# Performance work log

Measured on AMD Instinct MI355X. Metric: run time of the kernel, lower is better.

## Reference

```python
import jax, jax.numpy as jnp
import numpy as np

N, E, LE = 200000, 1000000, 1000000
ND, ED = 128, 128
EPS = 1e-5


def layer_norm(v, g, b):
    m = v.mean(-1, keepdims=True)
    var = ((v - m) ** 2).mean(-1, keepdims=True)
    return (v - m) * jax.lax.rsqrt(var + EPS) * g + b


def setup_inputs() -> dict:
    key = jax.random.key(0)
    ks = jax.random.split(key, 12)
    s = 0.02
    return {
        "x": jax.random.normal(ks[0], (N, ND), jnp.float32),
        "edge_attr": jax.random.normal(ks[1], (E, ED), jnp.float32),
        "lg_x": jax.random.normal(ks[2], (E, ED), jnp.float32),
        "lg_edge_attr": jax.random.normal(ks[3], (LE, 1), jnp.float32),
        "W_line": jax.random.normal(ks[4], (2 * ED + 1, ED), jnp.float32) * s,
        "b_line": jnp.zeros((ED,), jnp.float32),
        "W_gate": jax.random.normal(ks[5], (ED, ED), jnp.float32) * s,
        "b_gate": jnp.zeros((ED,), jnp.float32),
        "W_atom": jax.random.normal(ks[6], (ND + ED, ND), jnp.float32) * s,
        "b_atom": jnp.zeros((ND,), jnp.float32),
        "g_node": jnp.ones((ND,), jnp.float32),
        "beta_node": jnp.zeros((ND,), jnp.float32),
        "g_edge": jnp.ones((ED,), jnp.float32),
        "beta_edge": jnp.zeros((ED,), jnp.float32),
        "edge_index": jax.random.randint(ks[7], (2, E), 0, N, jnp.int64),
        "lg_edge_index": jax.random.randint(ks[8], (2, LE), 0, E, jnp.int64),
    }


def reference(x, edge_attr, lg_x, lg_edge_attr, W_line, b_line, W_gate, b_gate,
              W_atom, b_atom, g_node, beta_node, g_edge, beta_edge,
              edge_index, lg_edge_index):
    n_lg = lg_x.shape[0]  # == E (line-graph nodes are bonds)
    lg_src, lg_dst = lg_edge_index[0], lg_edge_index[1]
    # 1) LineGraphConv: gather-concat-MLP-scatter(mean)
    msg = jnp.concatenate([lg_x[lg_src], lg_x[lg_dst], lg_edge_attr], axis=-1)  # [LE, 2*ED+1]
    msg = jax.nn.silu(msg @ W_line + b_line)  # [LE, ED]
    agg_sum = jax.ops.segment_sum(msg, lg_dst, num_segments=n_lg)
    cnt = jax.ops.segment_sum(jnp.ones((lg_dst.shape[0], 1), msg.dtype), lg_dst, num_segments=n_lg)
    lg_x_new = lg_x + agg_sum / jnp.maximum(cnt, 1.0)  # scatter-mean, empty segs -> 0
    # 2) EdgeGateUpdate
    edge_attr_new = layer_norm(edge_attr + lg_x_new, g_edge, beta_edge)
    gate = jax.nn.sigmoid(edge_attr_new @ W_gate + b_gate)
    # 3) AtomGraphConv: gated scatter(sum) into atoms
    col = edge_index[1]
    agg = jax.ops.segment_sum(gate * edge_attr_new, col, num_segments=x.shape[0])  # [N, ED]
    h = jax.nn.silu(jnp.concatenate([x, agg], axis=-1) @ W_atom + b_atom)
    x_new = layer_norm(x + h, g_node, beta_node)
    return x_new, edge_attr_new, lg_x_new
```

## Files before the change

### kernel.cpp

```cpp
#include <hip/hip_runtime.h>


typedef __attribute__((ext_vector_type(8))) short s16x8;
typedef __attribute__((ext_vector_type(4))) float f32x4;

#define SCAN_CHUNK 2048

__device__ __forceinline__ short f2bf(float f) {
    unsigned u = __float_as_uint(f);
    u += 0x7FFF + ((u >> 16) & 1);
    return (short)(u >> 16);
}
__device__ __forceinline__ float bf2f(unsigned short h) {
    return __uint_as_float(((unsigned)h) << 16);
}
__device__ __forceinline__ s16x8 pack8(const float* v) {
    s16x8 r;
    #pragma unroll
    for (int j = 0; j < 8; ++j) r[j] = f2bf(v[j]);
    return r;
}

__global__ __launch_bounds__(256) void k_pack(const float* __restrict__ W,
                                              short* __restrict__ P, int nchunk) {
    int c = blockIdx.x * 256 + threadIdx.x;
    if (c >= nchunk) return;
    int g = c >> 7, col = c & 127, k0 = g * 8;
    s16x8 v;
    #pragma unroll
    for (int j = 0; j < 8; ++j) v[j] = f2bf(W[(size_t)(k0 + j) * 128 + col]);
    ((s16x8*)P)[c] = v;
}

__global__ __launch_bounds__(256) void k_cvt(const float* __restrict__ x,
                                             short* __restrict__ y, long n8) {
    long i = (long)blockIdx.x * 256 + threadIdx.x;
    const long stride = (long)gridDim.x * 256;
    for (; i < n8; i += stride) {
        float buf[8];
        *(float4*)&buf[0] = ((const float4*)x)[2 * i];
        *(float4*)&buf[4] = ((const float4*)x)[2 * i + 1];
        ((s16x8*)y)[i] = pack8(buf);
    }
}

__global__ __launch_bounds__(256) void k_hist(const int* __restrict__ idx,
                                              int* __restrict__ deg, int n) {
    int i = blockIdx.x * 256 + threadIdx.x;
    if (i < n) atomicAdd(&deg[idx[i]], 1);
}

__global__ __launch_bounds__(256) void k_scan_block(const int* __restrict__ in, int n,
                                                    int* __restrict__ out,
                                                    int* __restrict__ bsum) {
    __shared__ int ts[256];
    const int b = blockIdx.x, t = threadIdx.x;
    const int base = b * SCAN_CHUNK + t * 8;
    int v[8]; int s = 0;
    #pragma unroll
    for (int i = 0; i < 8; ++i) { v[i] = (base + i < n) ? in[base + i] : 0; s += v[i]; }
    ts[t] = s;
    __syncthreads();
    int x = s;
    for (int off = 1; off < 256; off <<= 1) {
        int y = (t >= off) ? ts[t - off] : 0;
        __syncthreads();
        x += y; ts[t] = x;
        __syncthreads();
    }
    if (t == 255) bsum[b] = x;
    int run = x - s;
    #pragma unroll
    for (int i = 0; i < 8; ++i) {
        if (base + i < n) out[base + i] = run;
        run += v[i];
    }
}

__global__ void k_scan_bsum(int* __restrict__ bsum, int nb) {
    const int lane = threadIdx.x;
    int carry = 0;
    for (int base = 0; base < nb; base += 64) {
        int i = base + lane;
        int v = (i < nb) ? bsum[i] : 0;
        int inc = v;
        #pragma unroll
        for (int off = 1; off < 64; off <<= 1) {
            int t = __shfl_up(inc, off);
            if (lane >= off) inc += t;
        }
        if (i < nb) bsum[i] = inc - v + carry;
        carry += __shfl(inc, 63);
    }
}

__global__ __launch_bounds__(256) void k_scan_add(int* __restrict__ off,
                                                  const int* __restrict__ bsum,
                                                  int n, int nedge) {
    int i = blockIdx.x * 256 + threadIdx.x;
    if (i < n) off[i] += bsum[i / SCAN_CHUNK];
    if (i == 0) off[n] = nedge;
}

__global__ __launch_bounds__(256) void k_fill_pos(const int* __restrict__ idx,
                                                  const int* __restrict__ off,
                                                  int* __restrict__ cur,
                                                  int* __restrict__ pos, int n) {
    int i = blockIdx.x * 256 + threadIdx.x;
    if (i < n) {
        int s = idx[i];
        int p = atomicAdd(&cur[s], 1);
        pos[i] = off[s] + p;
    }
}

__global__ __launch_bounds__(256) void k_line_csr(
    const short* __restrict__ lgx_bf, const float* __restrict__ lg_ea,
    const short* __restrict__ Wp, const float* __restrict__ W_line,
    const float* __restrict__ b_line,
    const int* __restrict__ lg_src, const int* __restrict__ lg_dst,
    const int* __restrict__ pos_lg,
    short* __restrict__ msg, int LEn)
{
    __shared__ __align__(16) short sh[128][136];
    const int tid = threadIdx.x;
    const int ln = tid & 63, wv = tid >> 6;
    const int l15 = ln & 15, lhi = ln >> 4;
    const int eb = blockIdx.x * 128 + wv * 32;
    const s16x8* Bv = (const s16x8*)Wp;

    const short *sp[2], *dp[2];
    #pragma unroll
    for (int mt = 0; mt < 2; ++mt) {
        int e = eb + mt * 16 + l15;
        int ec = e < LEn ? e : LEn - 1;
        sp[mt] = lgx_bf + (size_t)lg_src[ec] * 128;
        dp[mt] = lgx_bf + (size_t)lg_dst[ec] * 128;
    }

    f32x4 acc[2][8];
    #pragma unroll
    for (int m = 0; m < 2; ++m)
        #pragma unroll
        for (int n = 0; n < 8; ++n) acc[m][n] = (f32x4){0.f, 0.f, 0.f, 0.f};

    #pragma unroll 2
    for (int kt = 0; kt < 8; ++kt) {
        int ko = (kt & 3) * 32 + lhi * 8;
        s16x8 a[2];
        #pragma unroll
        for (int mt = 0; mt < 2; ++mt)
            a[mt] = *(const s16x8*)(((kt < 4) ? sp[mt] : dp[mt]) + ko);
        const s16x8* brow = Bv + (size_t)(kt * 4 + lhi) * 128 + l15;
        #pragma unroll
        for (int nt = 0; nt < 8; ++nt) {
            s16x8 b = brow[nt * 16];
            acc[0][nt] = __builtin_amdgcn_mfma_f32_16x16x32_bf16(a[0], b, acc[0][nt], 0, 0, 0);
            acc[1][nt] = __builtin_amdgcn_mfma_f32_16x16x32_bf16(a[1], b, acc[1][nt], 0, 0, 0);
        }
    }

    float eav[2][4];
    #pragma unroll
    for (int mt = 0; mt < 2; ++mt)
        #pragma unroll
        for (int r = 0; r < 4; ++r) {
            int e = eb + mt * 16 + lhi * 4 + r;
            eav[mt][r] = lg_ea[e < LEn ? e : 0];
        }

    #pragma unroll
    for (int nt = 0; nt < 8; ++nt) {
        int col = nt * 16 + l15;
        float wl = W_line[(size_t)256 * 128 + col];
        float bs = b_line[col];
        #pragma unroll
        for (int mt = 0; mt < 2; ++mt)
            #pragma unroll
            for (int r = 0; r < 4; ++r) {
                float v = acc[mt][nt][r] + bs + wl * eav[mt][r];
                float s = v / (1.f + __expf(-v));
                sh[wv * 32 + mt * 16 + lhi * 4 + r][col] = f2bf(s);
            }
    }
    __syncthreads();
    #pragma unroll
    for (int i = 0; i < 8; ++i) {
        int c = tid + i * 256;
        int row = c >> 4, q = c & 15;
        int e = blockIdx.x * 128 + row;
        if (e < LEn) {
            int p = pos_lg[e];
            *(s16x8*)&msg[(size_t)p * 128 + q * 8] = *(const s16x8*)&sh[row][q * 8];
        }
    }
}

__global__ __launch_bounds__(256) void k_lg_edge_fused(
    const short* __restrict__ msg, const float* __restrict__ lg_x,
    const float* __restrict__ edge_attr, const int* __restrict__ off,
    const float* __restrict__ g_edge, const float* __restrict__ beta_edge,
    float* __restrict__ out_lg, float* __restrict__ out_edge,
    short* __restrict__ enew_bf, int En)
{
    const int wave = threadIdx.x >> 6, lane = threadIdx.x & 63;
    const int e = blockIdx.x * 4 + wave;
    if (e >= En) return;
    const int o0 = off[e], o1 = off[e + 1];
    const int cnt = o1 - o0;
    const short* base = msg + (size_t)o0 * 128 + lane * 2;
    float s0 = 0.f, s1 = 0.f;
    int j = 0;
    for (; j + 1 < cnt; j += 2) {
        ushort2 u0 = *(const ushort2*)(base + (size_t)j * 128);
        ushort2 u1 = *(const ushort2*)(base + (size_t)(j + 1) * 128);
        s0 += bf2f(u0.x) + bf2f(u1.x);
        s1 += bf2f(u0.y) + bf2f(u1.y);
    }
    if (j < cnt) {
        ushort2 u = *(const ushort2*)(base + (size_t)j * 128);
        s0 += bf2f(u.x); s1 += bf2f(u.y);
    }
    const float inv = 1.f / fmaxf((float)cnt, 1.f);
    const size_t rb = (size_t)e * 128 + lane * 2;
    float2 lx = *(const float2*)&lg_x[rb];
    float l0 = fmaf(s0, inv, lx.x), l1 = fmaf(s1, inv, lx.y);
    *(float2*)&out_lg[rb] = make_float2(l0, l1);

    float2 ea = *(const float2*)&edge_attr[rb];
    float t0 = ea.x + l0, t1 = ea.y + l1;
    float s = t0 + t1, sq = t0 * t0 + t1 * t1;
    #pragma unroll
    for (int o = 32; o; o >>= 1) {
        s  += __shfl_xor(s, o);
        sq += __shfl_xor(sq, o);
    }
    float mean = s * (1.f / 128.f);
    float var  = sq * (1.f / 128.f) - mean * mean;
    float r = rsqrtf(var + 1e-5f);
    int j0 = lane * 2;
    float e0 = (t0 - mean) * r * g_edge[j0]     + beta_edge[j0];
    float e1 = (t1 - mean) * r * g_edge[j0 + 1] + beta_edge[j0 + 1];
    *(float2*)&out_edge[rb] = make_float2(e0, e1);
    if (enew_bf) {
        ushort2 ub = make_ushort2((unsigned short)f2bf(e0), (unsigned short)f2bf(e1));
        *(ushort2*)&enew_bf[rb] = ub;
    }
}

__global__ __launch_bounds__(256) void k_lg_gather(
    const short* __restrict__ msg, const float* __restrict__ lg_x,
    const int* __restrict__ off, float* __restrict__ out_lg, int En)
{
    const int wave = threadIdx.x >> 6, lane = threadIdx.x & 63;
    const int e = blockIdx.x * 4 + wave;
    if (e >= En) return;
    const int o0 = off[e], o1 = off[e + 1];
    const int cnt = o1 - o0;
    const short* base = msg + (size_t)o0 * 128 + lane * 2;
    float s0 = 0.f, s1 = 0.f;
    for (int j = 0; j < cnt; ++j) {
        ushort2 u = *(const ushort2*)(base + (size_t)j * 128);
        s0 += bf2f(u.x); s1 += bf2f(u.y);
    }
    const float inv = 1.f / fmaxf((float)cnt, 1.f);
    const size_t rb = (size_t)e * 128 + lane * 2;
    float2 lx = *(const float2*)&lg_x[rb];
    *(float2*)&out_lg[rb] = make_float2(fmaf(s0, inv, lx.x), fmaf(s1, inv, lx.y));
}

__global__ __launch_bounds__(256) void k_edge_ln(
    const float* __restrict__ lnew, const float* __restrict__ edge_attr,
    const float* __restrict__ g_edge, const float* __restrict__ beta_edge,
    float* __restrict__ out_edge, int En)
{
    const int wave = threadIdx.x >> 6, lane = threadIdx.x & 63;
    const int e = blockIdx.x * 4 + wave;
    if (e >= En) return;
    const size_t rb = (size_t)e * 128 + lane * 2;
    float2 lv = *(const float2*)&lnew[rb];
    float2 ea = *(const float2*)&edge_attr[rb];
    float t0 = ea.x + lv.x, t1 = ea.y + lv.y;
    float s = t0 + t1, sq = t0 * t0 + t1 * t1;
    #pragma unroll
    for (int o = 32; o; o >>= 1) { s += __shfl_xor(s, o); sq += __shfl_xor(sq, o); }
    float mean = s * (1.f / 128.f);
    float var  = sq * (1.f / 128.f) - mean * mean;
    float r = rsqrtf(var + 1e-5f);
    int j0 = lane * 2;
    float o0 = (t0 - mean) * r * g_edge[j0]     + beta_edge[j0];
    float o1 = (t1 - mean) * r * g_edge[j0 + 1] + beta_edge[j0 + 1];
    *(float2*)&out_edge[rb] = make_float2(o0, o1);
}

template <bool BF>
__global__ __launch_bounds__(256) void k_gate_csr(
    const short* __restrict__ EinB, const float* __restrict__ EinF,
    const short* __restrict__ Wp, const float* __restrict__ bg,
    const int* __restrict__ pos_at, short* __restrict__ gated, int En)
{
    __shared__ __align__(16) short sh[128][136];
    const int tid = threadIdx.x;
    const int ln = tid & 63, wv = tid >> 6;
    const int l15 = ln & 15, lhi = ln >> 4;
    const int eb = blockIdx.x * 128 + wv * 32;
    const s16x8* Bv = (const s16x8*)Wp;

    int rowi[2];
    #pragma unroll
    for (int mt = 0; mt < 2; ++mt) {
        int e = eb + mt * 16 + l15;
        rowi[mt] = e < En ? e : En - 1;
    }

    f32x4 acc[2][8];
    #pragma unroll
    for (int m = 0; m < 2; ++m)
        #pragma unroll
        for (int n = 0; n < 8; ++n) acc[m][n] = (f32x4){0.f, 0.f, 0.f, 0.f};

    #pragma unroll 2
    for (int kt = 0; kt < 4; ++kt) {
        int ko = kt * 32 + lhi * 8;
        s16x8 a[2];
        #pragma unroll
        for (int mt = 0; mt < 2; ++mt) {
            if (BF) {
                a[mt] = *(const s16x8*)(EinB + (size_t)rowi[mt] * 128 + ko);
            } else {
                const float* p = EinF + (size_t)rowi[mt] * 128 + ko;
                float buf[8];
                *(float4*)&buf[0] = *(const float4*)p;
                *(float4*)&buf[4] = *(const float4*)(p + 4);
                a[mt] = pack8(buf);
            }
        }
        const s16x8* brow = Bv + (size_t)(kt * 4 + lhi) * 128 + l15;
        #pragma unroll
        for (int nt = 0; nt < 8; ++nt) {
            s16x8 b = brow[nt * 16];
            acc[0][nt] = __builtin_amdgcn_mfma_f32_16x16x32_bf16(a[0], b, acc[0][nt], 0, 0, 0);
            acc[1][nt] = __builtin_amdgcn_mfma_f32_16x16x32_bf16(a[1], b, acc[1][nt], 0, 0, 0);
        }
    }

    #pragma unroll
    for (int nt = 0; nt < 8; ++nt) {
        int col = nt * 16 + l15;
        float bs = bg[col];
        #pragma unroll
        for (int mt = 0; mt < 2; ++mt)
            #pragma unroll
            for (int r = 0; r < 4; ++r) {
                int e = eb + mt * 16 + lhi * 4 + r;
                int ec = e < En ? e : En - 1;
                float g = 1.f / (1.f + __expf(-(acc[mt][nt][r] + bs)));
                float ev = BF ? bf2f(((const unsigned short*)EinB)[(size_t)ec * 128 + col])
                              : EinF[(size_t)ec * 128 + col];
                sh[wv * 32 + mt * 16 + lhi * 4 + r][col] = f2bf(g * ev);
            }
    }
    __syncthreads();
    #pragma unroll
    for (int i = 0; i < 8; ++i) {
        int c = tid + i * 256;
        int row = c >> 4, q = c & 15;
        int e = blockIdx.x * 128 + row;
        if (e < En) {
            int p = pos_at[e];
            *(s16x8*)&gated[(size_t)p * 128 + q * 8] = *(const s16x8*)&sh[row][q * 8];
        }
    }
}

__global__ __launch_bounds__(256) void k_atom_gather(
    const short* __restrict__ gated, const int* __restrict__ off,
    float* __restrict__ agg, int Nn)
{
    const int wave = threadIdx.x >> 6, lane = threadIdx.x & 63;
    const int n = blockIdx.x * 4 + wave;
    if (n >= Nn) return;
    const int o0 = off[n], o1 = off[n + 1];
    const int cnt = o1 - o0;
    const short* base = gated + (size_t)o0 * 128 + lane * 2;
    float s0 = 0.f, s1 = 0.f;
    int j = 0;
    for (; j + 1 < cnt; j += 2) {
        ushort2 u0 = *(const ushort2*)(base + (size_t)j * 128);
        ushort2 u1 = *(const ushort2*)(base + (size_t)(j + 1) * 128);
        s0 += bf2f(u0.x) + bf2f(u1.x);
        s1 += bf2f(u0.y) + bf2f(u1.y);
    }
    if (j < cnt) {
        ushort2 u = *(const ushort2*)(base + (size_t)j * 128);
        s0 += bf2f(u.x); s1 += bf2f(u.y);
    }
    *(float2*)&agg[(size_t)n * 128 + lane * 2] = make_float2(s0, s1);
}

__global__ __launch_bounds__(256) void k_atom_mfma(
    const float* __restrict__ x, const float* __restrict__ aggin,
    const short* __restrict__ Wp, const float* __restrict__ ba,
    const float* __restrict__ gn, const float* __restrict__ bn,
    float* __restrict__ out, int Nn)
{
    const int tid = threadIdx.x;
    const int ln = tid & 63, wv = tid >> 6;
    const int l15 = ln & 15, lhi = ln >> 4;
    const int nb = blockIdx.x * 128 + wv * 32;
    const s16x8* Bv = (const s16x8*)Wp;

    const float *xp[2], *ap[2];
    #pragma unroll
    for (int mt = 0; mt < 2; ++mt) {
        int n = nb + mt * 16 + l15;
        size_t nc = (size_t)(n < Nn ? n : Nn - 1) * 128;
        xp[mt] = x + nc;
        ap[mt] = aggin + nc;
    }

    f32x4 acc[2][8];
    #pragma unroll
    for (int m = 0; m < 2; ++m)
        #pragma unroll
        for (int n = 0; n < 8; ++n) acc[m][n] = (f32x4){0.f, 0.f, 0.f, 0.f};

    #pragma unroll 2
    for (int kt = 0; kt < 8; ++kt) {
        int ko = (kt & 3) * 32 + lhi * 8;
        s16x8 a[2];
        #pragma unroll
        for (int mt = 0; mt < 2; ++mt) {
            const float* p = ((kt < 4) ? xp[mt] : ap[mt]) + ko;
            float buf[8];
            *(float4*)&buf[0] = *(const float4*)p;
            *(float4*)&buf[4] = *(const float4*)(p + 4);
            a[mt] = pack8(buf);
        }
        const s16x8* brow = Bv + (size_t)(kt * 4 + lhi) * 128 + l15;
        #pragma unroll
        for (int nt = 0; nt < 8; ++nt) {
            s16x8 b = brow[nt * 16];
            acc[0][nt] = __builtin_amdgcn_mfma_f32_16x16x32_bf16(a[0], b, acc[0][nt], 0, 0, 0);
            acc[1][nt] = __builtin_amdgcn_mfma_f32_16x16x32_bf16(a[1], b, acc[1][nt], 0, 0, 0);
        }
    }

    #pragma unroll
    for (int mt = 0; mt < 2; ++mt)
        #pragma unroll
        for (int r = 0; r < 4; ++r) {
            int n = nb + mt * 16 + lhi * 4 + r;
            size_t nr = (size_t)(n < Nn ? n : 0) * 128;
            float s = 0.f, sq = 0.f;
            #pragma unroll
            for (int nt = 0; nt < 8; ++nt) {
                int col = nt * 16 + l15;
                float v = acc[mt][nt][r] + ba[col];
                float h = v / (1.f + __expf(-v));
                float t = x[nr + col] + h;
                acc[mt][nt][r] = t;
                s += t; sq += t * t;
            }
            #pragma unroll
            for (int off = 8; off; off >>= 1) {
                s  += __shfl_xor(s, off);
                sq += __shfl_xor(sq, off);
            }
            float mean = s * (1.f / 128.f);
            float var  = sq * (1.f / 128.f) - mean * mean;
            float rstd = rsqrtf(var + 1e-5f);
            if (n < Nn) {
                #pragma unroll
                for (int nt = 0; nt < 8; ++nt) {
                    int col = nt * 16 + l15;
                    float o = (acc[mt][nt][r] - mean) * rstd * gn[col] + bn[col];
                    out[(size_t)n * 128 + col] = o;
                }
            }
        }
}

extern "C" void kernel_launch(void* const* d_in, const int* in_sizes, int n_in,
                              void* d_out, int out_size, void* d_ws, size_t ws_size,
                              hipStream_t stream) {
    const float* x          = (const float*)d_in[0];
    const float* edge_attr  = (const float*)d_in[1];
    const float* lg_x       = (const float*)d_in[2];
    const float* lg_ea      = (const float*)d_in[3];
    const float* W_line     = (const float*)d_in[4];
    const float* b_line     = (const float*)d_in[5];
    const float* W_gate     = (const float*)d_in[6];
    const float* b_gate     = (const float*)d_in[7];
    const float* W_atom     = (const float*)d_in[8];
    const float* b_atom     = (const float*)d_in[9];
    const float* g_node     = (const float*)d_in[10];
    const float* beta_node  = (const float*)d_in[11];
    const float* g_edge     = (const float*)d_in[12];
    const float* beta_edge  = (const float*)d_in[13];
    const int*   edge_index    = (const int*)d_in[14];
    const int*   lg_edge_index = (const int*)d_in[15];

    const int Nn  = in_sizes[0] / 128;
    const int En  = in_sizes[1] / 128;
    const int LEn = in_sizes[3];

    float* out_x    = (float*)d_out;
    float* out_edge = out_x + (size_t)Nn * 128;
    float* out_lg   = out_edge + (size_t)En * 128;

    const int* lg_src = lg_edge_index;
    const int* lg_dst = lg_edge_index + LEn;
    const int* col    = edge_index + En;

    short* wp_line = (short*)d_ws;
    short* wp_gate = wp_line + 32768;
    short* wp_atom = wp_gate + 16384;
    int* ip = (int*)(wp_atom + 32768);
    int* off_lg  = ip;  ip += En + 1;
    int* deg_lg  = ip;  ip += En;
    int* cur_lg  = ip;  ip += En;
    int* pos_lg  = ip;  ip += LEn;
    int* bsum_lg = ip;  ip += 1024;
    int* off_at  = ip;  ip += Nn + 1;
    int* deg_at  = ip;  ip += Nn;
    int* cur_at  = ip;  ip += Nn;
    int* pos_at  = ip;  ip += En;
    int* bsum_at = ip;  ip += 1024;
    short* lgx_bf = (short*)(((uintptr_t)ip + 15) & ~(uintptr_t)15);
    short* bufA   = lgx_bf + (size_t)En * 128;
    const size_t need_B = ((uintptr_t)bufA) - (uintptr_t)d_ws;
    const size_t need_A = need_B + (size_t)En * 128 * 2;
    const bool tierA = ws_size >= need_A;

    hipMemsetAsync(deg_lg, 0, (size_t)En * 4, stream);
    hipMemsetAsync(cur_lg, 0, (size_t)En * 4, stream);
    hipMemsetAsync(deg_at, 0, (size_t)Nn * 4, stream);
    hipMemsetAsync(cur_at, 0, (size_t)Nn * 4, stream);

    k_pack<<<16, 256, 0, stream>>>(W_line, wp_line, 4096);
    k_pack<<<8,  256, 0, stream>>>(W_gate, wp_gate, 2048);
    k_pack<<<16, 256, 0, stream>>>(W_atom, wp_atom, 4096);
    k_cvt<<<2048, 256, 0, stream>>>(lg_x, lgx_bf, (long)En * 16);

    k_hist<<<(LEn + 255) / 256, 256, 0, stream>>>(lg_dst, deg_lg, LEn);
    k_hist<<<(En + 255) / 256, 256, 0, stream>>>(col, deg_at, En);
    const int nb_lg = (En + SCAN_CHUNK - 1) / SCAN_CHUNK;
    const int nb_at = (Nn + SCAN_CHUNK - 1) / SCAN_CHUNK;
    k_scan_block<<<nb_lg, 256, 0, stream>>>(deg_lg, En, off_lg, bsum_lg);
    k_scan_block<<<nb_at, 256, 0, stream>>>(deg_at, Nn, off_at, bsum_at);
    k_scan_bsum<<<1, 64, 0, stream>>>(bsum_lg, nb_lg);
    k_scan_bsum<<<1, 64, 0, stream>>>(bsum_at, nb_at);
    k_scan_add<<<(En + 255) / 256, 256, 0, stream>>>(off_lg, bsum_lg, En, LEn);
    k_scan_add<<<(Nn + 255) / 256, 256, 0, stream>>>(off_at, bsum_at, Nn, En);
    k_fill_pos<<<(LEn + 255) / 256, 256, 0, stream>>>(lg_dst, off_lg, cur_lg, pos_lg, LEn);
    k_fill_pos<<<(En + 255) / 256, 256, 0, stream>>>(col, off_at, cur_at, pos_at, En);

    if (tierA) {
        short* msg = bufA;
        k_line_csr<<<(LEn + 127) / 128, 256, 0, stream>>>(
            lgx_bf, lg_ea, wp_line, W_line, b_line, lg_src, lg_dst, pos_lg, msg, LEn);
        short* enew_bf = lgx_bf;
        k_lg_edge_fused<<<(En + 3) / 4, 256, 0, stream>>>(
            msg, lg_x, edge_attr, off_lg, g_edge, beta_edge,
            out_lg, out_edge, enew_bf, En);
        short* gated = bufA;
        k_gate_csr<true><<<(En + 127) / 128, 256, 0, stream>>>(
            enew_bf, nullptr, wp_gate, b_gate, pos_at, gated, En);
        k_atom_gather<<<(Nn + 3) / 4, 256, 0, stream>>>(gated, off_at, out_x, Nn);
    } else {
        short* msg = (short*)out_edge;
        k_line_csr<<<(LEn + 127) / 128, 256, 0, stream>>>(
            lgx_bf, lg_ea, wp_line, W_line, b_line, lg_src, lg_dst, pos_lg, msg, LEn);
        k_lg_gather<<<(En + 3) / 4, 256, 0, stream>>>(msg, lg_x, off_lg, out_lg, En);
        k_edge_ln<<<(En + 3) / 4, 256, 0, stream>>>(
            out_lg, edge_attr, g_edge, beta_edge, out_edge, En);
        short* gated = lgx_bf;
        k_gate_csr<false><<<(En + 127) / 128, 256, 0, stream>>>(
            nullptr, out_edge, wp_gate, b_gate, pos_at, gated, En);
        k_atom_gather<<<(Nn + 3) / 4, 256, 0, stream>>>(gated, off_at, out_x, Nn);
    }
    k_atom_mfma<<<(Nn + 127) / 128, 256, 0, stream>>>(
        x, out_x, wp_atom, b_atom, g_node, beta_node, out_x, Nn);
}
```

Measured before the change: 1.640 ms.

## Merge setup kernels, use bf16 residual/aggregate, half-wave vectorized gathers

Pairs of preprocessing kernels (weight pack, histogram, scans, scan-add, fill_pos) are merged into single launches, and the four memsets become two. The lg/edge fused kernel and the atom gather now process two rows per wave with 8-byte loads, and they launch twice as many rows per block. The lg_x residual is read from the existing bf16 copy instead of fp32. In the main path the atom aggregate is stored in bf16 and fed straight into the atom MFMA. Together these cut launch overhead and memory traffic. The cost is extra bf16 rounding in out_lg and in the aggregate, and a larger workspace requirement for the fast path.

After: 1.536 ms. 1.07x faster.

```diff
diff --git a/kernel.cpp b/kernel.cpp
--- a/kernel.cpp
+++ b/kernel.cpp
@@ -21,15 +21,22 @@
     return r;
 }
 
-__global__ __launch_bounds__(256) void k_pack(const float* __restrict__ W,
-                                              short* __restrict__ P, int nchunk) {
+__global__ __launch_bounds__(256) void k_pack3(
+    const float* __restrict__ Wl, const float* __restrict__ Wg,
+    const float* __restrict__ Wa,
+    short* __restrict__ Pl, short* __restrict__ Pg, short* __restrict__ Pa)
+{
     int c = blockIdx.x * 256 + threadIdx.x;
-    if (c >= nchunk) return;
-    int g = c >> 7, col = c & 127, k0 = g * 8;
+    const float* W; short* P; int cc;
+    if (c < 4096)       { W = Wl; P = Pl; cc = c; }
+    else if (c < 6144)  { W = Wg; P = Pg; cc = c - 4096; }
+    else if (c < 10240) { W = Wa; P = Pa; cc = c - 6144; }
+    else return;
+    int g = cc >> 7, col = cc & 127, k0 = g * 8;
     s16x8 v;
     #pragma unroll
     for (int j = 0; j < 8; ++j) v[j] = f2bf(W[(size_t)(k0 + j) * 128 + col]);
-    ((s16x8*)P)[c] = v;
+    ((s16x8*)P)[cc] = v;
 }
 
 __global__ __launch_bounds__(256) void k_cvt(const float* __restrict__ x,
@@ -44,17 +51,25 @@
     }
 }
 
-__global__ __launch_bounds__(256) void k_hist(const int* __restrict__ idx,
-                                              int* __restrict__ deg, int n) {
+__global__ __launch_bounds__(256) void k_hist2(
+    const int* __restrict__ idx1, int* __restrict__ deg1, int n1,
+    const int* __restrict__ idx2, int* __restrict__ deg2, int n2)
+{
     int i = blockIdx.x * 256 + threadIdx.x;
-    if (i < n) atomicAdd(&deg[idx[i]], 1);
-}
-
-__global__ __launch_bounds__(256) void k_scan_block(const int* __restrict__ in, int n,
-                                                    int* __restrict__ out,
-                                                    int* __restrict__ bsum) {
+    if (i < n1) atomicAdd(&deg1[idx1[i]], 1);
+    if (i < n2) atomicAdd(&deg2[idx2[i]], 1);
+}
+
+__global__ __launch_bounds__(256) void k_scan_block2(
+    const int* __restrict__ in1, int n1, int* __restrict__ out1, int* __restrict__ bsum1, int nb1,
+    const int* __restrict__ in2, int n2, int* __restrict__ out2, int* __restrict__ bsum2)
+{
     __shared__ int ts[256];
-    const int b = blockIdx.x, t = threadIdx.x;
+    int b = blockIdx.x;
+    const int* in; int n; int* out; int* bsum;
+    if (b < nb1) { in = in1; n = n1; out = out1; bsum = bsum1; }
+    else         { in = in2; n = n2; out = out2; bsum = bsum2; b -= nb1; }
+    const int t = threadIdx.x;
     const int base = b * SCAN_CHUNK + t * 8;
     int v[8]; int s = 0;
     #pragma unroll
@@ -77,8 +92,11 @@
     }
 }
 
-__global__ void k_scan_bsum(int* __restrict__ bsum, int nb) {
-    const int lane = threadIdx.x;
+__global__ void k_scan_bsum2(int* __restrict__ b1, int nb1,
+                             int* __restrict__ b2, int nb2) {
+    const int lane = threadIdx.x & 63;
+    int* bsum = (threadIdx.x < 64) ? b1 : b2;
+    const int nb  = (threadIdx.x < 64) ? nb1 : nb2;
     int carry = 0;
     for (int base = 0; base < nb; base += 64) {
         int i = base + lane;
@@ -94,23 +112,32 @@
     }
 }
 
-__global__ __launch_bounds__(256) void k_scan_add(int* __restrict__ off,
-                                                  const int* __restrict__ bsum,
-                                                  int n, int nedge) {
+__global__ __launch_bounds__(256) void k_scan_add2(
+    int* __restrict__ off1, const int* __restrict__ bsum1, int n1, int ne1,
+    int* __restrict__ off2, const int* __restrict__ bsum2, int n2, int ne2)
+{
     int i = blockIdx.x * 256 + threadIdx.x;
-    if (i < n) off[i] += bsum[i / SCAN_CHUNK];
-    if (i == 0) off[n] = nedge;
-}
-
-__global__ __launch_bounds__(256) void k_fill_pos(const int* __restrict__ idx,
-                                                  const int* __restrict__ off,
-                                                  int* __restrict__ cur,
-                                                  int* __restrict__ pos, int n) {
+    if (i < n1) off1[i] += bsum1[i / SCAN_CHUNK];
+    if (i < n2) off2[i] += bsum2[i / SCAN_CHUNK];
+    if (i == 0) { off1[n1] = ne1; off2[n2] = ne2; }
+}
+
+__global__ __launch_bounds__(256) void k_fill_pos2(
+    const int* __restrict__ idx1, const int* __restrict__ off1,
+    int* __restrict__ cur1, int* __restrict__ pos1, int n1,
+    const int* __restrict__ idx2, const int* __restrict__ off2,
+    int* __restrict__ cur2, int* __restrict__ pos2, int n2)
+{
     int i = blockIdx.x * 256 + threadIdx.x;
-    if (i < n) {
-        int s = idx[i];
-        int p = atomicAdd(&cur[s], 1);
-        pos[i] = off[s] + p;
+    if (i < n1) {
+        int s = idx1[i];
+        int p = atomicAdd(&cur1[s], 1);
+        pos1[i] = off1[s] + p;
+    }
+    if (i < n2) {
+        int s = idx2[i];
+        int p = atomicAdd(&cur2[s], 1);
+        pos2[i] = off2[s] + p;
     }
 }
 
@@ -197,54 +224,57 @@
 }
 
 __global__ __launch_bounds__(256) void k_lg_edge_fused(
-    const short* __restrict__ msg, const float* __restrict__ lg_x,
+    const short* __restrict__ msg, const short* __restrict__ lgx_bf,
     const float* __restrict__ edge_attr, const int* __restrict__ off,
     const float* __restrict__ g_edge, const float* __restrict__ beta_edge,
     float* __restrict__ out_lg, float* __restrict__ out_edge,
     short* __restrict__ enew_bf, int En)
 {
     const int wave = threadIdx.x >> 6, lane = threadIdx.x & 63;
-    const int e = blockIdx.x * 4 + wave;
+    const int half = lane >> 5, l = lane & 31;
+    const int e = blockIdx.x * 8 + wave * 2 + half;
     if (e >= En) return;
     const int o0 = off[e], o1 = off[e + 1];
     const int cnt = o1 - o0;
-    const short* base = msg + (size_t)o0 * 128 + lane * 2;
-    float s0 = 0.f, s1 = 0.f;
-    int j = 0;
-    for (; j + 1 < cnt; j += 2) {
-        ushort2 u0 = *(const ushort2*)(base + (size_t)j * 128);
-        ushort2 u1 = *(const ushort2*)(base + (size_t)(j + 1) * 128);
-        s0 += bf2f(u0.x) + bf2f(u1.x);
-        s1 += bf2f(u0.y) + bf2f(u1.y);
-    }
-    if (j < cnt) {
-        ushort2 u = *(const ushort2*)(base + (size_t)j * 128);
-        s0 += bf2f(u.x); s1 += bf2f(u.y);
+    const short* mbase = msg + (size_t)o0 * 128 + l * 4;
+    float s0 = 0.f, s1 = 0.f, s2 = 0.f, s3 = 0.f;
+    for (int j = 0; j < cnt; ++j) {
+        ushort4 u = *(const ushort4*)(mbase + (size_t)j * 128);
+        s0 += bf2f(u.x); s1 += bf2f(u.y); s2 += bf2f(u.z); s3 += bf2f(u.w);
     }
     const float inv = 1.f / fmaxf((float)cnt, 1.f);
-    const size_t rb = (size_t)e * 128 + lane * 2;
-    float2 lx = *(const float2*)&lg_x[rb];
-    float l0 = fmaf(s0, inv, lx.x), l1 = fmaf(s1, inv, lx.y);
-    *(float2*)&out_lg[rb] = make_float2(l0, l1);
-
-    float2 ea = *(const float2*)&edge_attr[rb];
-    float t0 = ea.x + l0, t1 = ea.y + l1;
-    float s = t0 + t1, sq = t0 * t0 + t1 * t1;
-    #pragma unroll
-    for (int o = 32; o; o >>= 1) {
+    const size_t rb = (size_t)e * 128 + l * 4;
+    ushort4 lxu = *(const ushort4*)&lgx_bf[rb];
+    float l0 = fmaf(s0, inv, bf2f(lxu.x));
+    float l1 = fmaf(s1, inv, bf2f(lxu.y));
+    float l2 = fmaf(s2, inv, bf2f(lxu.z));
+    float l3 = fmaf(s3, inv, bf2f(lxu.w));
+    *(float4*)&out_lg[rb] = make_float4(l0, l1, l2, l3);
+
+    float4 ea = *(const float4*)&edge_attr[rb];
+    float t0 = ea.x + l0, t1 = ea.y + l1, t2 = ea.z + l2, t3 = ea.w + l3;
+    float s = t0 + t1 + t2 + t3;
+    float sq = t0 * t0 + t1 * t1 + t2 * t2 + t3 * t3;
+    #pragma unroll
+    for (int o = 16; o; o >>= 1) {
         s  += __shfl_xor(s, o);
         sq += __shfl_xor(sq, o);
     }
     float mean = s * (1.f / 128.f);
     float var  = sq * (1.f / 128.f) - mean * mean;
     float r = rsqrtf(var + 1e-5f);
-    int j0 = lane * 2;
-    float e0 = (t0 - mean) * r * g_edge[j0]     + beta_edge[j0];
-    float e1 = (t1 - mean) * r * g_edge[j0 + 1] + beta_edge[j0 + 1];
-    *(float2*)&out_edge[rb] = make_float2(e0, e1);
+    int j0 = l * 4;
+    float4 gg = *(const float4*)&g_edge[j0];
+    float4 bb = *(const float4*)&beta_edge[j0];
+    float e0 = fmaf((t0 - mean) * r, gg.x, bb.x);
+    float e1 = fmaf((t1 - mean) * r, gg.y, bb.y);
+    float e2 = fmaf((t2 - mean) * r, gg.z, bb.z);
+    float e3 = fmaf((t3 - mean) * r, gg.w, bb.w);
+    *(float4*)&out_edge[rb] = make_float4(e0, e1, e2, e3);
     if (enew_bf) {
-        ushort2 ub = make_ushort2((unsigned short)f2bf(e0), (unsigned short)f2bf(e1));
-        *(ushort2*)&enew_bf[rb] = ub;
+        ushort4 ub = make_ushort4((unsigned short)f2bf(e0), (unsigned short)f2bf(e1),
+                                  (unsigned short)f2bf(e2), (unsigned short)f2bf(e3));
+        *(ushort4*)&enew_bf[rb] = ub;
     }
 }
 
@@ -373,33 +403,37 @@
     }
 }
 
+template <bool BF_OUT>
 __global__ __launch_bounds__(256) void k_atom_gather(
     const short* __restrict__ gated, const int* __restrict__ off,
-    float* __restrict__ agg, int Nn)
+    float* __restrict__ aggf, short* __restrict__ aggb, int Nn)
 {
     const int wave = threadIdx.x >> 6, lane = threadIdx.x & 63;
-    const int n = blockIdx.x * 4 + wave;
+    const int half = lane >> 5, l = lane & 31;
+    const int n = blockIdx.x * 8 + wave * 2 + half;
     if (n >= Nn) return;
     const int o0 = off[n], o1 = off[n + 1];
     const int cnt = o1 - o0;
-    const short* base = gated + (size_t)o0 * 128 + lane * 2;
-    float s0 = 0.f, s1 = 0.f;
-    int j = 0;
-    for (; j + 1 < cnt; j += 2) {
-        ushort2 u0 = *(const ushort2*)(base + (size_t)j * 128);
-        ushort2 u1 = *(const ushort2*)(base + (size_t)(j + 1) * 128);
-        s0 += bf2f(u0.x) + bf2f(u1.x);
-        s1 += bf2f(u0.y) + bf2f(u1.y);
-    }
-    if (j < cnt) {
-        ushort2 u = *(const ushort2*)(base + (size_t)j * 128);
-        s0 += bf2f(u.x); s1 += bf2f(u.y);
-    }
-    *(float2*)&agg[(size_t)n * 128 + lane * 2] = make_float2(s0, s1);
-}
-
+    const short* base = gated + (size_t)o0 * 128 + l * 4;
+    float s0 = 0.f, s1 = 0.f, s2 = 0.f, s3 = 0.f;
+    for (int j = 0; j < cnt; ++j) {
+        ushort4 u = *(const ushort4*)(base + (size_t)j * 128);
+        s0 += bf2f(u.x); s1 += bf2f(u.y); s2 += bf2f(u.z); s3 += bf2f(u.w);
+    }
+    const size_t rb = (size_t)n * 128 + l * 4;
+    if (BF_OUT) {
+        ushort4 ub = make_ushort4((unsigned short)f2bf(s0), (unsigned short)f2bf(s1),
+                                  (unsigned short)f2bf(s2), (unsigned short)f2bf(s3));
+        *(ushort4*)&aggb[rb] = ub;
+    } else {
+        *(float4*)&aggf[rb] = make_float4(s0, s1, s2, s3);
+    }
+}
+
+template <bool AGGBF>
 __global__ __launch_bounds__(256) void k_atom_mfma(
-    const float* __restrict__ x, const float* __restrict__ aggin,
+    const float* __restrict__ x, const float* __restrict__ aggf,
+    const short* __restrict__ aggb,
     const short* __restrict__ Wp, const float* __restrict__ ba,
     const float* __restrict__ gn, const float* __restrict__ bn,
     float* __restrict__ out, int Nn)
@@ -410,13 +444,13 @@
     const int nb = blockIdx.x * 128 + wv * 32;
     const s16x8* Bv = (const s16x8*)Wp;
 
-    const float *xp[2], *ap[2];
+    const float* xp[2];
+    size_t nc[2];
     #pragma unroll
     for (int mt = 0; mt < 2; ++mt) {
         int n = nb + mt * 16 + l15;
-        size_t nc = (size_t)(n < Nn ? n : Nn - 1) * 128;
-        xp[mt] = x + nc;
-        ap[mt] = aggin + nc;
+        nc[mt] = (size_t)(n < Nn ? n : Nn - 1) * 128;
+        xp[mt] = x + nc[mt];
     }
 
     f32x4 acc[2][8];
@@ -431,11 +465,21 @@
         s16x8 a[2];
         #pragma unroll
         for (int mt = 0; mt < 2; ++mt) {
-            const float* p = ((kt < 4) ? xp[mt] : ap[mt]) + ko;
-            float buf[8];
-            *(float4*)&buf[0] = *(const float4*)p;
-            *(float4*)&buf[4] = *(const float4*)(p + 4);
-            a[mt] = pack8(buf);
+            if (kt < 4) {
+                const float* p = xp[mt] + ko;
+                float buf[8];
+                *(float4*)&buf[0] = *(const float4*)p;
+                *(float4*)&buf[4] = *(const float4*)(p + 4);
+                a[mt] = pack8(buf);
+            } else if (AGGBF) {
+                a[mt] = *(const s16x8*)(aggb + nc[mt] + ko);
+            } else {
+                const float* p = aggf + nc[mt] + ko;
+                float buf[8];
+                *(float4*)&buf[0] = *(const float4*)p;
+                *(float4*)&buf[4] = *(const float4*)(p + 4);
+                a[mt] = pack8(buf);
+            }
         }
         const s16x8* brow = Bv + (size_t)(kt * 4 + lhi) * 128 + l15;
         #pragma unroll
@@ -529,45 +573,45 @@
     int* bsum_at = ip;  ip += 1024;
     short* lgx_bf = (short*)(((uintptr_t)ip + 15) & ~(uintptr_t)15);
     short* bufA   = lgx_bf + (size_t)En * 128;
+    short* agg_bf = bufA + (size_t)En * 128;
     const size_t need_B = ((uintptr_t)bufA) - (uintptr_t)d_ws;
-    const size_t need_A = need_B + (size_t)En * 128 * 2;
+    const size_t need_A = ((uintptr_t)(agg_bf + (size_t)Nn * 128)) - (uintptr_t)d_ws;
     const bool tierA = ws_size >= need_A;
 
-    hipMemsetAsync(deg_lg, 0, (size_t)En * 4, stream);
-    hipMemsetAsync(cur_lg, 0, (size_t)En * 4, stream);
-    hipMemsetAsync(deg_at, 0, (size_t)Nn * 4, stream);
-    hipMemsetAsync(cur_at, 0, (size_t)Nn * 4, stream);
-
-    k_pack<<<16, 256, 0, stream>>>(W_line, wp_line, 4096);
-    k_pack<<<8,  256, 0, stream>>>(W_gate, wp_gate, 2048);
-    k_pack<<<16, 256, 0, stream>>>(W_atom, wp_atom, 4096);
+    hipMemsetAsync(deg_lg, 0, (size_t)En * 8, stream);
+    hipMemsetAsync(deg_at, 0, (size_t)Nn * 8, stream);
+
+    k_pack3<<<40, 256, 0, stream>>>(W_line, W_gate, W_atom, wp_line, wp_gate, wp_atom);
     k_cvt<<<2048, 256, 0, stream>>>(lg_x, lgx_bf, (long)En * 16);
 
-    k_hist<<<(LEn + 255) / 256, 256, 0, stream>>>(lg_dst, deg_lg, LEn);
-    k_hist<<<(En + 255) / 256, 256, 0, stream>>>(col, deg_at, En);
+    const int nmax = LEn > En ? LEn : En;
+    k_hist2<<<(nmax + 255) / 256, 256, 0, stream>>>(lg_dst, deg_lg, LEn, col, deg_at, En);
     const int nb_lg = (En + SCAN_CHUNK - 1) / SCAN_CHUNK;
     const int nb_at = (Nn + SCAN_CHUNK - 1) / SCAN_CHUNK;
-    k_scan_block<<<nb_lg, 256, 0, stream>>>(deg_lg, En, off_lg, bsum_lg);
-    k_scan_block<<<nb_at, 256, 0, stream>>>(deg_at, Nn, off_at, bsum_at);
-    k_scan_bsum<<<1, 64, 0, stream>>>(bsum_lg, nb_lg);
-    k_scan_bsum<<<1, 64, 0, stream>>>(bsum_at, nb_at);
-    k_scan_add<<<(En + 255) / 256, 256, 0, stream>>>(off_lg, bsum_lg, En, LEn);
-    k_scan_add<<<(Nn + 255) / 256, 256, 0, stream>>>(off_at, bsum_at, Nn, En);
-    k_fill_pos<<<(LEn + 255) / 256, 256, 0, stream>>>(lg_dst, off_lg, cur_lg, pos_lg, LEn);
-    k_fill_pos<<<(En + 255) / 256, 256, 0, stream>>>(col, off_at, cur_at, pos_at, En);
+    k_scan_block2<<<nb_lg + nb_at, 256, 0, stream>>>(
+        deg_lg, En, off_lg, bsum_lg, nb_lg, deg_at, Nn, off_at, bsum_at);
+    k_scan_bsum2<<<1, 128, 0, stream>>>(bsum_lg, nb_lg, bsum_at, nb_at);
+    const int sa_max = En > Nn ? En : Nn;
+    k_scan_add2<<<(sa_max + 255) / 256, 256, 0, stream>>>(
+        off_lg, bsum_lg, En, LEn, off_at, bsum_at, Nn, En);
+    k_fill_pos2<<<(nmax + 255) / 256, 256, 0, stream>>>(
+        lg_dst, off_lg, cur_lg, pos_lg, LEn, col, off_at, cur_at, pos_at, En);
 
     if (tierA) {
         short* msg = bufA;
         k_line_csr<<<(LEn + 127) / 128, 256, 0, stream>>>(
             lgx_bf, lg_ea, wp_line, W_line, b_line, lg_src, lg_dst, pos_lg, msg, LEn);
         short* enew_bf = lgx_bf;
-        k_lg_edge_fused<<<(En + 3) / 4, 256, 0, stream>>>(
-            msg, lg_x, edge_attr, off_lg, g_edge, beta_edge,
+        k_lg_edge_fused<<<(En + 7) / 8, 256, 0, stream>>>(
+            msg, lgx_bf, edge_attr, off_lg, g_edge, beta_edge,
             out_lg, out_edge, enew_bf, En);
         short* gated = bufA;
         k_gate_csr<true><<<(En + 127) / 128, 256, 0, stream>>>(
             enew_bf, nullptr, wp_gate, b_gate, pos_at, gated, En);
-        k_atom_gather<<<(Nn + 3) / 4, 256, 0, stream>>>(gated, off_at, out_x, Nn);
+        k_atom_gather<true><<<(Nn + 7) / 8, 256, 0, stream>>>(
+            gated, off_at, nullptr, agg_bf, Nn);
+        k_atom_mfma<true><<<(Nn + 127) / 128, 256, 0, stream>>>(
+            x, nullptr, agg_bf, wp_atom, b_atom, g_node, beta_node, out_x, Nn);
     } else {
         short* msg = (short*)out_edge;
         k_line_csr<<<(LEn + 127) / 128, 256, 0, stream>>>(
@@ -578,8 +622,9 @@
         short* gated = lgx_bf;
         k_gate_csr<false><<<(En + 127) / 128, 256, 0, stream>>>(
             nullptr, out_edge, wp_gate, b_gate, pos_at, gated, En);
-        k_atom_gather<<<(Nn + 3) / 4, 256, 0, stream>>>(gated, off_at, out_x, Nn);
-    }
-    k_atom_mfma<<<(Nn + 127) / 128, 256, 0, stream>>>(
-        x, out_x, wp_atom, b_atom, g_node, beta_node, out_x, Nn);
-}
+        k_atom_gather<false><<<(Nn + 7) / 8, 256, 0, stream>>>(
+            gated, off_at, out_x, nullptr, Nn);
+        k_atom_mfma<false><<<(Nn + 127) / 128, 256, 0, stream>>>(
+            x, out_x, nullptr, wp_atom, b_atom, g_node, beta_node, out_x, Nn);
+    }
+}
```
